# Kernel optimization log

Hardware: AMD Instinct MI355X
Metric: run time of the kernel (lower is better)

## Reference

```python
import jax, jax.numpy as jnp
import numpy as np

NUM_CLASSES = 80
IGNORE_THRESH = 0.7
COORD_SCALE = 1.0
NOOBJ_SCALE = 1.0
OBJ_SCALE = 5.0
CLASS_SCALE = 1.0
NUM_A = 3  # anchors per scale


def iou_cxcywh(a, b):
    """Elementwise/broadcast IoU for boxes in (cx, cy, w, h) format."""
    tl = jnp.maximum(a[..., :2] - a[..., 2:] * 0.5, b[..., :2] - b[..., 2:] * 0.5)
    br = jnp.minimum(a[..., :2] + a[..., 2:] * 0.5, b[..., :2] + b[..., 2:] * 0.5)
    wh = jnp.clip(br - tl, 0.0)
    inter = wh[..., 0] * wh[..., 1]
    union = a[..., 2] * a[..., 3] + b[..., 2] * b[..., 3] - inter
    return inter / union


def yolo_scale_loss(out, targets, anchors):
    B, C, H, W = out.shape
    A, nc = NUM_A, NUM_CLASSES
    HW = H * W
    # ---------------- target building (on detached outputs) ----------------
    od = jax.lax.stop_gradient(out).reshape(B, A, 5 + nc, H, W).transpose(0, 1, 3, 4, 2)  # B,A,H,W,85
    xs = jnp.arange(W, dtype=out.dtype)
    ys = jnp.arange(H, dtype=out.dtype)
    px = jax.nn.sigmoid(od[..., 0]) + xs[None, None, None, :]
    py = jax.nn.sigmoid(od[..., 1]) + ys[None, None, :, None]
    pw = jnp.exp(od[..., 2]) * anchors[:, 0][None, :, None, None]
    ph = jnp.exp(od[..., 3]) * anchors[:, 1][None, :, None, None]
    pred = jnp.stack([px, py, pw, ph], -1).transpose(0, 2, 3, 1, 4)  # B,H,W,A,4
    pred = pred.reshape(B, HW, A, 4)

    Y, X = jnp.meshgrid(jnp.arange(H, dtype=out.dtype), jnp.arange(W, dtype=out.dtype), indexing='ij')
    cell = jnp.stack([X, Y], -1).reshape(HW, 1, 2)  # cell corner (x1y1)
    anc_x1y1 = jnp.concatenate([jnp.broadcast_to(cell, (HW, A, 2)),
                                jnp.broadcast_to(anchors[None], (HW, A, 2))], -1)  # HW,A,4
    anc_xcyc = anc_x1y1.at[..., :2].add(0.5)

    valid = targets.sum(axis=2) > 0  # [B,K] padded-front object mask
    num_obj = valid.sum(axis=1)
    K = targets.shape[1]
    gt = targets[..., :4] * jnp.array([W, H, W, H], dtype=out.dtype)  # grid units
    gt_cls = targets[..., 4].astype(jnp.int32)

    # IoU of every prediction vs every gt: [B, HW*A, K]
    ious = iou_cxcywh(pred.reshape(B, HW * A, 1, 4), gt[:, None, :, :])
    ious = jnp.where(valid[:, None, :], ious, -1.0)
    max_iou = ious.max(-1).reshape(B, HW, A)

    has_pos = (max_iou > IGNORE_THRESH).reshape(B, -1).any(axis=1)
    iou_mask = jnp.full((B, HW, A), NOOBJ_SCALE, dtype=out.dtype)
    iou_mask = jnp.where(has_pos[:, None, None] & (max_iou >= IGNORE_THRESH), 0.0, iou_mask)
    iou_mask = jnp.where((num_obj > 0)[:, None, None], iou_mask, 0.0)

    # per-object responsible cell + anchor
    cx = jnp.clip(jnp.floor(gt[..., 0]), 0, W - 1).astype(jnp.int32)  # [B,K]
    cy = jnp.clip(jnp.floor(gt[..., 1]), 0, H - 1).astype(jnp.int32)
    cell_idx = cy * W + cx
    a_boxes = anc_xcyc[cell_idx]  # [B,K,A,4]
    ov = iou_cxcywh(a_boxes, gt[:, :, None, :])  # [B,K,A]
    a_star = jnp.argmax(ov, -1).astype(jnp.int32)  # [B,K]

    resp = anc_x1y1[cell_idx, a_star]  # [B,K,4] responsible anchor (x1,y1,w,h)
    delta = jnp.stack([gt[..., 0] - resp[..., 0], gt[..., 1] - resp[..., 1],
                       gt[..., 2] / resp[..., 2], gt[..., 3] / resp[..., 3]], -1)  # [B,K,4]
    bidx = jnp.arange(B, dtype=jnp.int32)[:, None]
    obj_iou = max_iou[bidx, cell_idx, a_star]  # [B,K]

    N = B * HW * A
    f = (jnp.arange(B, dtype=jnp.int32)[:, None] * (HW * A) + cell_idx * A + a_star)  # [B,K]
    rank = jnp.arange(B * K, dtype=jnp.int32).reshape(B, K)
    rank_m = jnp.where(valid, rank, -1)
    seg = jax.ops.segment_max(rank_m.ravel(), f.ravel(), num_segments=N)
    winner = valid & (rank == seg[f])
    f_eff = jnp.where(winner, f, N).ravel()  # losers -> dummy slot

    box_target = jnp.zeros((N + 1, 4), out.dtype).at[f_eff].set(delta.reshape(-1, 4))[:-1]
    box_mask = jnp.zeros(N + 1, out.dtype).at[f_eff].set(1.0)[:-1]
    class_target = jnp.zeros(N + 1, jnp.int32).at[f_eff].set(gt_cls.ravel())[:-1]
    class_mask = box_mask
    iou_target = jnp.zeros(N + 1, out.dtype).at[f_eff].set(obj_iou.ravel())[:-1]
    iou_mask = jnp.concatenate([iou_mask.ravel(), jnp.zeros(1, out.dtype)]).at[f_eff].set(OBJ_SCALE)[:-1]

    # ---------------- loss on live outputs ----------------
    o = out.reshape(B, A, 5 + nc, H, W).transpose(0, 3, 4, 1, 2).reshape(N, 5 + nc)
    pred_delta = jnp.concatenate([jax.nn.sigmoid(o[:, :2]), jnp.exp(o[:, 2:4])], axis=1)
    pred_conf = jax.nn.sigmoid(o[:, 4])
    logits = o[:, 5:]

    box_loss = jnp.sum(box_mask[:, None] * (pred_delta - box_target) ** 2)
    iou_loss = jnp.sum((pred_conf * iou_mask - iou_target * iou_mask) ** 2)
    lse = jax.nn.logsumexp(logits, axis=-1)
    tgt_logit = jnp.take_along_axis(logits, class_target[:, None], axis=1)[:, 0]
    class_loss = jnp.sum(class_mask * (lse - tgt_logit))

    return (box_loss * COORD_SCALE / 2.0 + iou_loss / 2.0 + class_loss * CLASS_SCALE) / B


def reference(o1, o2, o3, targets, anchors):
    # anchor_mask = [[6,7,8],[3,4,5],[0,1,2]]
    l1 = yolo_scale_loss(o1, targets, anchors[6:9])
    l2 = yolo_scale_loss(o2, targets, anchors[3:6])
    l3 = yolo_scale_loss(o3, targets, anchors[0:3])
    return (l1 + l2 + l3) / 3.0


def setup_inputs() -> dict:
    key = jax.random.key(0)
    ks = jax.random.split(key, 5)
    B, K, nc = 16, 50, 80
    o1 = jax.random.normal(ks[0], (B, 255, 13, 13), jnp.float32)
    o2 = jax.random.normal(ks[1], (B, 255, 26, 26), jnp.float32)
    o3 = jax.random.normal(ks[2], (B, 255, 52, 52), jnp.float32)
    boxes = jax.random.uniform(ks[3], (B, K, 4), jnp.float32, 0.05, 0.95)
    cls = jax.random.randint(ks[4], (B, K, 1), 0, nc).astype(jnp.float32)
    targets = jnp.concatenate([boxes, cls], axis=-1)
    anchors_px = np.array([[10, 13], [16, 30], [33, 23], [30, 61], [62, 45],
                           [59, 119], [116, 90], [156, 198], [373, 326]], np.float32)
    strides = np.array([8, 8, 8, 16, 16, 16, 32, 32, 32], np.float32)[:, None]
    anchors = jnp.asarray(anchors_px / strides)
    return {"o1": o1, "o2": o2, "o3": o3, "targets": targets, "anchors": anchors}
```

## Files before the change

### kernel.cpp

```cpp
#include <hip/hip_runtime.h>

static constexpr int Bn = 16, Kn = 50, NCn = 80;
static constexpr int NTOT = 16 * 3 * (169 + 676 + 2704);
static constexpr int NBLK_A = (NTOT + 255) / 256;
static constexpr int NBLK_ASSIGN = 12;
static constexpr int NREC = 3 * Bn * Kn;
static constexpr int NBLK_F = NREC / 4;
static constexpr int MIOU_OFF = 0;
static constexpr int NO_OFF   = 170352;
static constexpr int REC_OFF  = 170368;
static constexpr int EXPC_OFF = 189568;
static constexpr int EXPD_OFF = 190240;
static constexpr int CNT_OFF  = 200896;
static constexpr int ACC_OFF  = 200897;
static constexpr float IGN = 0.7f;
static constexpr float W_BOX = 1.0f / 96.0f;
static constexpr float W_IOU = 1.0f / 96.0f;
static constexpr float W_CLS = 1.0f / 48.0f;

__device__ __forceinline__ float sigf(float x) { return 1.0f / (1.0f + __expf(-x)); }

__device__ __forceinline__ float iou_box(float ax, float ay, float aw, float ah,
                                         float bx, float by, float bw, float bh) {
  float tlx = fmaxf(ax - aw * 0.5f, bx - bw * 0.5f);
  float tly = fmaxf(ay - ah * 0.5f, by - bh * 0.5f);
  float brx = fminf(ax + aw * 0.5f, bx + bw * 0.5f);
  float bry = fminf(ay + ah * 0.5f, by + bh * 0.5f);
  float w = fmaxf(brx - tlx, 0.0f);
  float h = fmaxf(bry - tly, 0.0f);
  float inter = w * h;
  float uni = aw * ah + bw * bh - inter;
  return inter / uni;
}

__device__ __forceinline__ void decode_cell(int g, int& s, int& H, int& HW,
                                            int& base, int& b, int& a, int& hw) {
  if (g < 8112)       { s = 0; H = 13; HW = 169;  base = 0; }
  else if (g < 40560) { s = 1; H = 26; HW = 676;  base = 8112; }
  else                { s = 2; H = 52; HW = 2704; base = 40560; }
  int local = g - base;
  hw = local % HW;
  int t = local / HW;
  a = t % 3;
  b = t / 3;
}

__global__ __launch_bounds__(256) void kMain(const float* __restrict__ o0,
                                             const float* __restrict__ o1,
                                             const float* __restrict__ o2,
                                             const float* __restrict__ tgt,
                                             const float* __restrict__ anc,
                                             float* __restrict__ ws) {
  __shared__ float tg[Bn * Kn * 5];
  __shared__ float4 tga[Bn * Kn];
  __shared__ float  tgb[Bn * Kn];
  __shared__ float ls1[48], ls2[48], lhp[48];
  __shared__ int lcnt;
  int tid = threadIdx.x;

  if (blockIdx.x >= NBLK_A) {
    for (int i = tid; i < Bn * Kn * 5; i += 256) tg[i] = tgt[i];
    if (blockIdx.x == NBLK_A && tid == 0) {
      ((int*)ws)[CNT_OFF] = 0;
      ws[ACC_OFF] = 0.0f;
    }
    __syncthreads();
    int wv = (blockIdx.x - NBLK_A) * 4 + (tid >> 6);
    int lane = tid & 63;
    int s = wv / 16, b = wv % 16;
    int H, HW, base;
    if (s == 0)      { H = 13; HW = 169;  base = 0; }
    else if (s == 1) { H = 26; HW = 676;  base = 8112; }
    else             { H = 52; HW = 2704; base = 40560; }
    int W = H;
    int aoff = 6 - 3 * s;
    float aw0 = anc[aoff * 2],       ah0 = anc[aoff * 2 + 1];
    float aw1 = anc[(aoff + 1) * 2], ah1 = anc[(aoff + 1) * 2 + 1];
    float aw2 = anc[(aoff + 2) * 2], ah2 = anc[(aoff + 2) * 2 + 1];

    bool valid = false;
    int gslot = -1 - lane;
    float dx = 0, dy = 0, dw = 0, dh = 0, tc = 0;
    if (lane < Kn) {
      const float* tp = &tg[(b * Kn + lane) * 5];
      float tx = tp[0], ty = tp[1], tw = tp[2], th = tp[3];
      tc = tp[4];
      if (tx + ty + tw + th + tc > 0.0f) {
        valid = true;
        float gx = tx * W, gy = ty * H, gw = tw * W, gh = th * H;
        int cx = (int)floorf(gx); cx = min(max(cx, 0), W - 1);
        int cy = (int)floorf(gy); cy = min(max(cy, 0), H - 1);
        float ccx = cx + 0.5f, ccy = cy + 0.5f;
        float i0 = iou_box(ccx, ccy, aw0, ah0, gx, gy, gw, gh);
        float i1 = iou_box(ccx, ccy, aw1, ah1, gx, gy, gw, gh);
        float i2 = iou_box(ccx, ccy, aw2, ah2, gx, gy, gw, gh);
        int astar = 0; float bi = i0;
        if (i1 > bi) { bi = i1; astar = 1; }
        if (i2 > bi) { bi = i2; astar = 2; }
        float raw = (astar == 0) ? aw0 : (astar == 1) ? aw1 : aw2;
        float rah = (astar == 0) ? ah0 : (astar == 1) ? ah1 : ah2;
        gslot = base + (b * 3 + astar) * HW + cy * W + cx;
        dx = gx - (float)cx;
        dy = gy - (float)cy;
        dw = gw / raw;
        dh = gh / rah;
      }
    }
    bool win = valid;
    for (int k2 = 1; k2 < Kn; k2++) {
      int other = __shfl(gslot, k2);
      if (k2 > lane && other == gslot) win = false;
    }
    unsigned long long bal = __ballot(valid);
    if (lane == 0 && s == 0) ((int*)ws)[NO_OFF + b] = (int)__popcll(bal);
    if (lane < Kn) {
      float* r = ws + REC_OFF + (size_t)(wv * Kn + lane) * 8;
      r[0] = win ? 1.0f : 0.0f;
      r[1] = __int_as_float(gslot);
      r[2] = dx; r[3] = dy; r[4] = dw; r[5] = dh;
      r[6] = tc;
      r[7] = 0.0f;
    }
    return;
  }

  for (int i = tid; i < Bn * Kn; i += 256) {
    const float* tp = tgt + (size_t)i * 5;
    float tx = tp[0], ty = tp[1], tw = tp[2], th = tp[3], tc = tp[4];
    float hw_ = tw * 0.5f, hh_ = th * 0.5f;
    tga[i] = make_float4(tx - hw_, ty - hh_, tx + hw_, ty + hh_);
    tgb[i] = (tx + ty + tw + th + tc > 0.0f) ? tw * th : -1.0f;
  }
  if (tid < 48) { ls1[tid] = 0.0f; ls2[tid] = 0.0f; lhp[tid] = 0.0f; }
  if (tid == 0) lcnt = 0;
  __syncthreads();

  int g = blockIdx.x * 256 + tid;
  if (g < NTOT) {
    int s, H, HW, base, b, a, hw;
    decode_cell(g, s, H, HW, base, b, a, hw);
    int W = H;
    float Wf = (float)W, W2 = Wf * Wf;
    const float* o = (s == 0) ? o0 : (s == 1) ? o1 : o2;
    int x = hw % W, y = hw / W;
    int aoff = 6 - 3 * s;
    float aw = anc[(aoff + a) * 2], ah = anc[(aoff + a) * 2 + 1];
    int ob = (b * 255 + a * 85) * HW + hw;
    float px = sigf(o[ob]) + (float)x;
    float py = sigf(o[ob + HW]) + (float)y;
    float pw = __expf(o[ob + 2 * HW]) * aw;
    float ph = __expf(o[ob + 3 * HW]) * ah;
    float conf = sigf(o[ob + 4 * HW]);
    float pxl = px - pw * 0.5f, pxr = px + pw * 0.5f;
    float pyl = py - ph * 0.5f, pyr = py + ph * 0.5f;
    float parea = pw * ph;
    float bi = -1.0f, bu = 1.0f;
    const float4* ca = &tga[b * Kn];
    const float*  cb = &tgb[b * Kn];
    for (int k = 0; k < Kn; k++) {
      float fa = cb[k];
      if (fa >= 0.0f) {
        float4 c = ca[k];
        float tlx = fmaxf(pxl, c.x * Wf);
        float tly = fmaxf(pyl, c.y * Wf);
        float brx = fminf(pxr, c.z * Wf);
        float bry = fminf(pyr, c.w * Wf);
        float w = fmaxf(brx - tlx, 0.0f);
        float h = fmaxf(bry - tly, 0.0f);
        float inter = w * h;
        float uni = parea + fa * W2 - inter;
        if (inter * bu > bi * uni) { bi = inter; bu = uni; }
      }
    }
    float mi = bi / bu;
    ws[MIOU_OFF + g] = mi;
    int key = s * 16 + b;
    float c2 = conf * conf;
    atomicAdd(&ls1[key], c2);
    if (mi >= IGN) atomicAdd(&ls2[key], c2);
    if (mi > IGN) lhp[key] = 1.0f;
  }
  __syncthreads();
  if (tid < 48 && ls1[tid] != 0.0f) {
    int p = atomicAdd(&lcnt, 1);
    float* e = ws + EXPD_OFF + (size_t)blockIdx.x * 16 + p * 4;
    e[0] = __int_as_float(tid);
    e[1] = ls1[tid];
    e[2] = ls2[tid];
    e[3] = lhp[tid];
  }
  __syncthreads();
  if (tid == 0) ((int*)ws)[EXPC_OFF + blockIdx.x] = lcnt;
}

__global__ __launch_bounds__(256) void kFinal(const float* __restrict__ o0,
                                              const float* __restrict__ o1,
                                              const float* __restrict__ o2,
                                              float* __restrict__ ws,
                                              float* __restrict__ out) {
  __shared__ float wsum[4];
  __shared__ int amLast;
  __shared__ float S1L[48], S2L[48], HPL[48];
  int tid = threadIdx.x;
  int lane = tid & 63;
  int idx = (blockIdx.x * 256 + tid) >> 6;
  float contrib = 0.0f;

  const float* r = ws + REC_OFF + (size_t)idx * 8;
  if (r[0] != 0.0f) {
    int g = __float_as_int(r[1]);
    int s, H, HW, base, b, a, hw;
    decode_cell(g, s, H, HW, base, b, a, hw);
    const float* o = (s == 0) ? o0 : (s == 1) ? o1 : o2;
    int ob = (b * 255 + a * 85) * HW + hw;
    float l1 = (lane < NCn) ? o[ob + (5 + lane) * HW] : -1e30f;
    float l2 = (lane + 64 < NCn) ? o[ob + (5 + lane + 64) * HW] : -1e30f;
    float mx = fmaxf(l1, l2);
    for (int off = 32; off > 0; off >>= 1) mx = fmaxf(mx, __shfl_xor(mx, off));
    float sm = __expf(l1 - mx) + __expf(l2 - mx);
    for (int off = 32; off > 0; off >>= 1) sm += __shfl_xor(sm, off);
    if (lane == 0) {
      float lse = mx + __logf(sm);
      int cls = (int)r[6];
      float tgtl = o[ob + (5 + cls) * HW];
      float d0 = sigf(o[ob]) - r[2];
      float d1 = sigf(o[ob + HW]) - r[3];
      float d2 = __expf(o[ob + 2 * HW]) - r[4];
      float d3 = __expf(o[ob + 3 * HW]) - r[5];
      float box = d0 * d0 + d1 * d1 + d2 * d2 + d3 * d3;
      float conf = sigf(o[ob + 4 * HW]);
      float mi = ws[MIOU_OFF + g];
      float basem = (mi >= IGN) ? 0.0f : 1.0f;
      float vb = conf * basem;
      float dv = 5.0f * (conf - mi);
      float iouc = dv * dv - vb * vb;
      contrib += box * W_BOX + iouc * W_IOU + (lse - tgtl) * W_CLS;
    }
  }

  for (int off = 32; off > 0; off >>= 1) contrib += __shfl_down(contrib, off);
  if (lane == 0) wsum[tid >> 6] = contrib;
  __syncthreads();
  if (tid == 0) {
    float t = wsum[0] + wsum[1] + wsum[2] + wsum[3];
    if (t != 0.0f) atomicAdd(&ws[ACC_OFF], t);
    __threadfence();
    int ticket = atomicAdd((int*)ws + CNT_OFF, 1);
    amLast = (ticket == NBLK_F - 1);
  }
  __syncthreads();
  if (!amLast) return;

  __threadfence();
  if (tid < 48) { S1L[tid] = 0.0f; S2L[tid] = 0.0f; HPL[tid] = 0.0f; }
  __syncthreads();
  for (int bid = tid; bid < NBLK_A; bid += 256) {
    int cnt = ((const int*)ws)[EXPC_OFF + bid];
    const float* e = ws + EXPD_OFF + (size_t)bid * 16;
    for (int j = 0; j < cnt; j++) {
      int key = __float_as_int(e[j * 4]);
      atomicAdd(&S1L[key], e[j * 4 + 1]);
      atomicAdd(&S2L[key], e[j * 4 + 2]);
      if (e[j * 4 + 3] != 0.0f) HPL[key] = 1.0f;
    }
  }
  __syncthreads();
  float c = 0.0f;
  if (tid < 48) {
    int b = tid & 15;
    int nobj = ((const int*)ws)[NO_OFF + b];
    if (nobj > 0)
      c += ((HPL[tid] > 0.0f) ? (S1L[tid] - S2L[tid]) : S1L[tid]) * W_IOU;
  }
  for (int off = 32; off > 0; off >>= 1) c += __shfl_down(c, off);
  if (lane == 0) wsum[tid >> 6] = c;
  __syncthreads();
  if (tid == 0) {
    float fix = wsum[0] + wsum[1] + wsum[2] + wsum[3];
    float acc = atomicAdd(&ws[ACC_OFF], 0.0f);
    out[0] = acc + fix;
  }
}

extern "C" void kernel_launch(void* const* d_in, const int* in_sizes, int n_in,
                              void* d_out, int out_size, void* d_ws, size_t ws_size,
                              hipStream_t stream) {
  const float* o0  = (const float*)d_in[0];
  const float* o1  = (const float*)d_in[1];
  const float* o2  = (const float*)d_in[2];
  const float* tgt = (const float*)d_in[3];
  const float* anc = (const float*)d_in[4];
  float* ws  = (float*)d_ws;
  float* out = (float*)d_out;

  kMain<<<NBLK_A + NBLK_ASSIGN, 256, 0, stream>>>(o0, o1, o2, tgt, anc, ws);
  kFinal<<<NBLK_F, 256, 0, stream>>>(o0, o1, o2, ws, out);
}
```

Before: 127.2 us.

## Replace last-block atomic ticket reduction with separate single-block sum kernel

The final stage no longer uses a global atomic accumulator and a ticket counter to elect a last block; instead each kFinal block writes its partial sum to workspace, and a new single-block kSum kernel merges the per-block expansion records and the partials. kFinal blocks grow from 256 to 1024 threads, so there are a quarter as many blocks. This removes the atomics, thread fences and the counter initialisation in kMain, at the cost of one extra kernel launch and a serial tail kernel.

```diff
diff --git a/kernel.cpp b/kernel.cpp
--- a/kernel.cpp
+++ b/kernel.cpp
@@ -5,14 +5,13 @@
 static constexpr int NBLK_A = (NTOT + 255) / 256;
 static constexpr int NBLK_ASSIGN = 12;
 static constexpr int NREC = 3 * Bn * Kn;
-static constexpr int NBLK_F = NREC / 4;
+static constexpr int NBLK_F = NREC / 16;
 static constexpr int MIOU_OFF = 0;
 static constexpr int NO_OFF   = 170352;
 static constexpr int REC_OFF  = 170368;
 static constexpr int EXPC_OFF = 189568;
 static constexpr int EXPD_OFF = 190240;
-static constexpr int CNT_OFF  = 200896;
-static constexpr int ACC_OFF  = 200897;
+static constexpr int PARTF_OFF = 200896;
 static constexpr float IGN = 0.7f;
 static constexpr float W_BOX = 1.0f / 96.0f;
 static constexpr float W_IOU = 1.0f / 96.0f;
@@ -60,10 +59,6 @@
 
   if (blockIdx.x >= NBLK_A) {
     for (int i = tid; i < Bn * Kn * 5; i += 256) tg[i] = tgt[i];
-    if (blockIdx.x == NBLK_A && tid == 0) {
-      ((int*)ws)[CNT_OFF] = 0;
-      ws[ACC_OFF] = 0.0f;
-    }
     __syncthreads();
     int wv = (blockIdx.x - NBLK_A) * 4 + (tid >> 6);
     int lane = tid & 63;
@@ -193,17 +188,14 @@
   if (tid == 0) ((int*)ws)[EXPC_OFF + blockIdx.x] = lcnt;
 }
 
-__global__ __launch_bounds__(256) void kFinal(const float* __restrict__ o0,
-                                              const float* __restrict__ o1,
-                                              const float* __restrict__ o2,
-                                              float* __restrict__ ws,
-                                              float* __restrict__ out) {
-  __shared__ float wsum[4];
-  __shared__ int amLast;
-  __shared__ float S1L[48], S2L[48], HPL[48];
+__global__ __launch_bounds__(1024) void kFinal(const float* __restrict__ o0,
+                                               const float* __restrict__ o1,
+                                               const float* __restrict__ o2,
+                                               float* __restrict__ ws) {
+  __shared__ float wsum[16];
   int tid = threadIdx.x;
   int lane = tid & 63;
-  int idx = (blockIdx.x * 256 + tid) >> 6;
+  int idx = (blockIdx.x * 1024 + tid) >> 6;
   float contrib = 0.0f;
 
   const float* r = ws + REC_OFF + (size_t)idx * 8;
@@ -242,16 +234,18 @@
   if (lane == 0) wsum[tid >> 6] = contrib;
   __syncthreads();
   if (tid == 0) {
-    float t = wsum[0] + wsum[1] + wsum[2] + wsum[3];
-    if (t != 0.0f) atomicAdd(&ws[ACC_OFF], t);
-    __threadfence();
-    int ticket = atomicAdd((int*)ws + CNT_OFF, 1);
-    amLast = (ticket == NBLK_F - 1);
-  }
-  __syncthreads();
-  if (!amLast) return;
-
-  __threadfence();
+    float t = 0.0f;
+    #pragma unroll
+    for (int i = 0; i < 16; i++) t += wsum[i];
+    ws[PARTF_OFF + blockIdx.x] = t;
+  }
+}
+
+__global__ __launch_bounds__(256) void kSum(const float* __restrict__ ws,
+                                            float* __restrict__ out) {
+  __shared__ float S1L[48], S2L[48], HPL[48];
+  __shared__ float bsum[4];
+  int tid = threadIdx.x;
   if (tid < 48) { S1L[tid] = 0.0f; S2L[tid] = 0.0f; HPL[tid] = 0.0f; }
   __syncthreads();
   for (int bid = tid; bid < NBLK_A; bid += 256) {
@@ -272,14 +266,11 @@
     if (nobj > 0)
       c += ((HPL[tid] > 0.0f) ? (S1L[tid] - S2L[tid]) : S1L[tid]) * W_IOU;
   }
+  for (int i = tid; i < NBLK_F; i += 256) c += ws[PARTF_OFF + i];
   for (int off = 32; off > 0; off >>= 1) c += __shfl_down(c, off);
-  if (lane == 0) wsum[tid >> 6] = c;
-  __syncthreads();
-  if (tid == 0) {
-    float fix = wsum[0] + wsum[1] + wsum[2] + wsum[3];
-    float acc = atomicAdd(&ws[ACC_OFF], 0.0f);
-    out[0] = acc + fix;
-  }
+  if ((tid & 63) == 0) bsum[tid >> 6] = c;
+  __syncthreads();
+  if (tid == 0) out[0] = bsum[0] + bsum[1] + bsum[2] + bsum[3];
 }
 
 extern "C" void kernel_launch(void* const* d_in, const int* in_sizes, int n_in,
@@ -294,5 +285,6 @@
   float* out = (float*)d_out;
 
   kMain<<<NBLK_A + NBLK_ASSIGN, 256, 0, stream>>>(o0, o1, o2, tgt, anc, ws);
-  kFinal<<<NBLK_F, 256, 0, stream>>>(o0, o1, o2, ws, out);
-}
+  kFinal<<<NBLK_F, 1024, 0, stream>>>(o0, o1, o2, ws);
+  kSum<<<1, 256, 0, stream>>>(ws, out);
+}
```

Result: faster. 114.1 us, median of 2 (-10.3%).
